# Kernel tuning notes

Hardware: AMD Instinct MI355X
Metric: run time of the kernel (lower is better)

Reference implementation:

```python
import jax, jax.numpy as jnp
import numpy as np

DIM = 1024
NUM_HEADS = 16
HEAD_DIM = DIM // NUM_HEADS
SCALE = HEAD_DIM ** (-0.5)


def setup_inputs() -> dict:
    key = jax.random.key(0)
    ks = jax.random.split(key, 5)
    B, N, C = 2, 2048, DIM
    q = jax.random.normal(ks[0], (B, N, C), dtype=jnp.float32)
    k = jax.random.normal(ks[1], (B, N, C), dtype=jnp.float32)
    v = jax.random.normal(ks[2], (B, N, C), dtype=jnp.float32)
    # fused qkv Linear weight, torch layout [3*C, C]; no bias (qkv_bias=False)
    qkv_w = jax.random.normal(ks[3], (3 * C, C), dtype=jnp.float32) * (C ** -0.5)
    proj_w = jax.random.normal(ks[4], (C, C), dtype=jnp.float32) * (C ** -0.5)
    proj_b = jnp.zeros((C,), dtype=jnp.float32)
    return {"q": q, "k": k, "v": v, "qkv_w": qkv_w, "proj_w": proj_w,
            "proj_b": proj_b, "use_mask": 1}


def reference(q, k, v, qkv_w, proj_w, proj_b, use_mask):
    B, N, C = q.shape
    N_k = k.shape[1]
    H, hd = NUM_HEADS, HEAD_DIM
    # The original applies the full fused qkv Linear to each of q,k,v and keeps
    # only slice 0/1/2 respectively; computing just the used slice is identical math.
    wq, wk, wv = qkv_w[:C], qkv_w[C:2 * C], qkv_w[2 * C:]
    qh = (q @ wq.T).reshape(B, N, H, hd).transpose(0, 2, 1, 3)      # [B,H,N,hd]
    kh = (k @ wk.T).reshape(B, N_k, H, hd).transpose(0, 2, 1, 3)    # [B,H,Nk,hd]
    vh = (v @ wv.T).reshape(B, N_k, H, hd).transpose(0, 2, 1, 3)    # [B,H,Nk,hd]
    attn = jnp.einsum('bhnd,bhmd->bhnm', qh, kh) * SCALE            # [B,H,N,Nk]
    if use_mask:  # static Python flag -> causal tril mask as in the source
        msk = jnp.tril(jnp.ones((N, N_k), dtype=bool))
        attn = jnp.where(msk[None, None], attn, jnp.float32(-1e9))
    attn = jax.nn.softmax(attn, axis=-1)
    x = jnp.einsum('bhnm,bhmd->bhnd', attn, vh)                     # [B,H,N,hd]
    x = x.transpose(0, 2, 1, 3).reshape(B, N, C)
    x = x @ proj_w.T + proj_b
    return x, attn
```

## Files before the change

### kernel.cpp

```cpp
#include <hip/hip_runtime.h>


typedef unsigned short u16;
typedef unsigned int u32;
typedef __attribute__((ext_vector_type(8))) short s16x8;
typedef __attribute__((ext_vector_type(4))) float f32x4;
typedef __attribute__((ext_vector_type(4))) u16 u16x4;

#define AS1 __attribute__((address_space(1)))
#define AS3 __attribute__((address_space(3)))

static __device__ __forceinline__ u16 f2bf(float f) {
  u32 u = __builtin_bit_cast(u32, f);
  u = (u + 0x7fffu + ((u >> 16) & 1u)) >> 16;
  return (u16)u;
}

static __device__ __forceinline__ void gll16(const u16* g, u16* l) {
  __builtin_amdgcn_global_load_lds((const AS1 u32*)g, (AS3 u32*)l, 16, 0, 0);
}

static __device__ __forceinline__ f32x4 mfma_bf16(s16x8 a, s16x8 b, f32x4 c) {
  return __builtin_amdgcn_mfma_f32_16x16x32_bf16(a, b, c, 0, 0, 0);
}

__global__ __launch_bounds__(256) void cast_kernel(const float* __restrict__ in,
                                                   u16* __restrict__ out, int n4) {
  int i = blockIdx.x * 256 + threadIdx.x;
  if (i < n4) {
    f32x4 v = ((const f32x4*)in)[i];
    u16x4 o = { f2bf(v.x), f2bf(v.y), f2bf(v.z), f2bf(v.w) };
    ((u16x4*)out)[i] = o;
  }
}

static __device__ __forceinline__ void gemm_core_1024(
    const u16* __restrict__ A, const u16* __restrict__ Bm,
    int m0, int n0, int t, u16* a_s, u16* b_s, f32x4 acc[4][4]) {
  const int lane = t & 63;
  const int w = t >> 6;
  const int wm = (w & 1) * 64, wn = (w >> 1) * 64;
  const int lrow = lane & 15, lq = lane >> 4;
  const int r0 = t >> 2;
  const int c0 = (t & 3) * 8;

  for (int kt = 0; kt < 1024; kt += 32) {
    __syncthreads();
    gll16(A  + (size_t)(m0 + r0)      * 1024 + kt + c0, &a_s[(size_t)t * 8]);
    gll16(A  + (size_t)(m0 + r0 + 64) * 1024 + kt + c0, &a_s[(size_t)(t + 256) * 8]);
    gll16(Bm + (size_t)(n0 + r0)      * 1024 + kt + c0, &b_s[(size_t)t * 8]);
    gll16(Bm + (size_t)(n0 + r0 + 64) * 1024 + kt + c0, &b_s[(size_t)(t + 256) * 8]);
    __syncthreads();
    s16x8 af[4], bfr[4];
#pragma unroll
    for (int x = 0; x < 4; x++) af[x]  = *(const s16x8*)&a_s[(wm + x*16 + lrow)*32 + lq*8];
#pragma unroll
    for (int x = 0; x < 4; x++) bfr[x] = *(const s16x8*)&b_s[(wn + x*16 + lrow)*32 + lq*8];
#pragma unroll
    for (int tm = 0; tm < 4; tm++)
#pragma unroll
      for (int tn = 0; tn < 4; tn++)
        acc[tm][tn] = mfma_bf16(af[tm], bfr[tn], acc[tm][tn]);
  }
}

__global__ __launch_bounds__(256) void gemm_qkv_kernel(
    const u16* __restrict__ qb, const u16* __restrict__ kb, const u16* __restrict__ vb,
    const u16* __restrict__ wb, u16* __restrict__ Qh, u16* __restrict__ Kh,
    u16* __restrict__ Vt) {
  __shared__ u16 a_s[128*32], b_s[128*32];
  const int mode = blockIdx.z;
  const u16* A = (mode == 0) ? qb : (mode == 1) ? kb : vb;
  const u16* Bm = wb + (size_t)mode * (1024 * 1024);
  const int m0 = blockIdx.y * 128, n0 = blockIdx.x * 128;
  const int t = threadIdx.x;
  f32x4 acc[4][4];
  const f32x4 Z = {0.f, 0.f, 0.f, 0.f};
#pragma unroll
  for (int i = 0; i < 4; i++)
#pragma unroll
    for (int j = 0; j < 4; j++) acc[i][j] = Z;

  gemm_core_1024(A, Bm, m0, n0, t, a_s, b_s, acc);

  const int lane = t & 63, w = t >> 6;
  const int wm = (w & 1) * 64, wn = (w >> 1) * 64;
  const int lrow = lane & 15, lq = lane >> 4;
#pragma unroll
  for (int tm = 0; tm < 4; tm++) {
#pragma unroll
    for (int tn = 0; tn < 4; tn++) {
      const int ng = n0 + wn + tn * 16 + lrow;
      const int h = ng >> 6, d = ng & 63;
#pragma unroll
      for (int i = 0; i < 4; i++) {
        const int mg = m0 + wm + tm * 16 + lq * 4 + i;
        const int b = mg >> 11, s = mg & 2047;
        const float v = acc[tm][tn][i];
        if (mode == 0)
          Qh[((size_t)(b * 16 + h) * 2048 + s) * 64 + d] = f2bf(v * 0.125f);
        else if (mode == 1)
          Kh[((size_t)(b * 16 + h) * 2048 + s) * 64 + d] = f2bf(v);
        else
          Vt[((size_t)(b * 16 + h) * 64 + d) * 2048 + s] = f2bf(v);
      }
    }
  }
}

__global__ __launch_bounds__(256) void gemm_proj_kernel(
    const u16* __restrict__ xatt, const u16* __restrict__ pwb,
    const float* __restrict__ bias, float* __restrict__ out) {
  __shared__ u16 a_s[128*32], b_s[128*32];
  const int m0 = blockIdx.y * 128, n0 = blockIdx.x * 128;
  const int t = threadIdx.x;
  f32x4 acc[4][4];
  const f32x4 Z = {0.f, 0.f, 0.f, 0.f};
#pragma unroll
  for (int i = 0; i < 4; i++)
#pragma unroll
    for (int j = 0; j < 4; j++) acc[i][j] = Z;

  gemm_core_1024(xatt, pwb, m0, n0, t, a_s, b_s, acc);

  const int lane = t & 63, w = t >> 6;
  const int wm = (w & 1) * 64, wn = (w >> 1) * 64;
  const int lrow = lane & 15, lq = lane >> 4;
#pragma unroll
  for (int tn = 0; tn < 4; tn++) {
    const int ng = n0 + wn + tn * 16 + lrow;
    const float bv = bias[ng];
#pragma unroll
    for (int tm = 0; tm < 4; tm++) {
#pragma unroll
      for (int i = 0; i < 4; i++) {
        const int mg = m0 + wm + tm * 16 + lq * 4 + i;
        out[(size_t)mg * 1024 + ng] = acc[tm][tn][i] + bv;
      }
    }
  }
}

__global__ __launch_bounds__(256) void attn_kernel(
    const u16* __restrict__ Qh, const u16* __restrict__ Kh, const u16* __restrict__ Vt,
    float* __restrict__ attn, u16* __restrict__ xatt, const int* __restrict__ use_mask_p) {
  __shared__ u16 q_s[64*64], k_s[64*64], v_s[64*64];
  __shared__ u16 p_s[4][16*64];

  const int bh = blockIdx.y;
  const int q0 = blockIdx.x * 64;
  const int t = threadIdx.x;
  const int lane = t & 63, w = t >> 6;
  const int lrow = lane & 15, lq = lane >> 4;
  const int use_mask = *use_mask_p;
  const int T = use_mask ? (q0 >> 6) : 31;

  const int rs = t >> 3;
  const int cs = (t & 7) * 8;

  const u16* qg = Qh + ((size_t)bh * 2048 + q0) * 64;
  gll16(qg + (size_t)rs * 64 + cs,        &q_s[(size_t)t * 8]);
  gll16(qg + (size_t)(rs + 32) * 64 + cs, &q_s[(size_t)(t + 256) * 8]);
  __syncthreads();

  s16x8 qf[2];
#pragma unroll
  for (int kq = 0; kq < 2; kq++)
    qf[kq] = *(const s16x8*)&q_s[(w * 16 + lrow) * 64 + kq * 32 + lq * 8];

  const u16* kg = Kh + (size_t)bh * (2048 * 64);
  const u16* vg = Vt + (size_t)bh * (64 * 2048);

  float l_acc[4] = {0.f, 0.f, 0.f, 0.f};
  for (int tt = 0; tt <= T; tt++) {
    __syncthreads();
    gll16(kg + (size_t)(tt * 64 + rs) * 64 + cs,      &k_s[(size_t)t * 8]);
    gll16(kg + (size_t)(tt * 64 + rs + 32) * 64 + cs, &k_s[(size_t)(t + 256) * 8]);
    __syncthreads();
    f32x4 sacc[4];
    const f32x4 Z = {0.f, 0.f, 0.f, 0.f};
#pragma unroll
    for (int tn = 0; tn < 4; tn++) {
      sacc[tn] = Z;
#pragma unroll
      for (int kq = 0; kq < 2; kq++) {
        s16x8 kf = *(const s16x8*)&k_s[(tn * 16 + lrow) * 64 + kq * 32 + lq * 8];
        sacc[tn] = mfma_bf16(qf[kq], kf, sacc[tn]);
      }
    }
    const bool diag = use_mask && (tt == T);
    float part[4] = {0.f, 0.f, 0.f, 0.f};
#pragma unroll
    for (int tn = 0; tn < 4; tn++)
#pragma unroll
      for (int i = 0; i < 4; i++) {
        const bool ok = !diag || (tn * 16 + lrow <= w * 16 + lq * 4 + i);
        part[i] += ok ? __expf(sacc[tn][i]) : 0.f;
      }
#pragma unroll
    for (int i = 0; i < 4; i++) {
      float p = part[i];
      p += __shfl_xor(p, 1, 16);
      p += __shfl_xor(p, 2, 16);
      p += __shfl_xor(p, 4, 16);
      p += __shfl_xor(p, 8, 16);
      l_acc[i] += p;
    }
  }
  float inv_l[4];
#pragma unroll
  for (int i = 0; i < 4; i++) inv_l[i] = 1.0f / l_acc[i];

  f32x4 oacc[4];
  const f32x4 Z = {0.f, 0.f, 0.f, 0.f};
#pragma unroll
  for (int i = 0; i < 4; i++) oacc[i] = Z;

  for (int tt = 0; tt <= T; tt++) {
    __syncthreads();
    gll16(kg + (size_t)(tt * 64 + rs) * 64 + cs,      &k_s[(size_t)t * 8]);
    gll16(kg + (size_t)(tt * 64 + rs + 32) * 64 + cs, &k_s[(size_t)(t + 256) * 8]);
    gll16(vg + (size_t)rs * 2048 + tt * 64 + cs,        &v_s[(size_t)t * 8]);
    gll16(vg + (size_t)(rs + 32) * 2048 + tt * 64 + cs, &v_s[(size_t)(t + 256) * 8]);
    __syncthreads();
    f32x4 sacc[4];
#pragma unroll
    for (int tn = 0; tn < 4; tn++) {
      sacc[tn] = Z;
#pragma unroll
      for (int kq = 0; kq < 2; kq++) {
        s16x8 kf = *(const s16x8*)&k_s[(tn * 16 + lrow) * 64 + kq * 32 + lq * 8];
        sacc[tn] = mfma_bf16(qf[kq], kf, sacc[tn]);
      }
    }
    const bool diag = use_mask && (tt == T);
    float* abase = attn + ((size_t)(bh * 2048 + q0 + w * 16)) * 2048 + tt * 64;
#pragma unroll
    for (int tn = 0; tn < 4; tn++)
#pragma unroll
      for (int i = 0; i < 4; i++) {
        const bool ok = !diag || (tn * 16 + lrow <= w * 16 + lq * 4 + i);
        const float p = ok ? __expf(sacc[tn][i]) * inv_l[i] : 0.f;
        const int rl = lq * 4 + i;
        abase[(size_t)rl * 2048 + tn * 16 + lrow] = p;
        p_s[w][rl * 64 + tn * 16 + lrow] = f2bf(p);
      }
    s16x8 pf[2];
#pragma unroll
    for (int kq = 0; kq < 2; kq++)
      pf[kq] = *(const s16x8*)&p_s[w][lrow * 64 + kq * 32 + lq * 8];
#pragma unroll
    for (int td = 0; td < 4; td++)
#pragma unroll
      for (int kq = 0; kq < 2; kq++) {
        s16x8 vf = *(const s16x8*)&v_s[(td * 16 + lrow) * 64 + kq * 32 + lq * 8];
        oacc[td] = mfma_bf16(pf[kq], vf, oacc[td]);
      }
  }

  const int b = bh >> 4, h = bh & 15;
#pragma unroll
  for (int td = 0; td < 4; td++)
#pragma unroll
    for (int i = 0; i < 4; i++) {
      const int row = q0 + w * 16 + lq * 4 + i;
      xatt[((size_t)(b * 2048 + row)) * 1024 + h * 64 + td * 16 + lrow] = f2bf(oacc[td][i]);
    }

  if (use_mask) {
    const int zc0 = q0 + 64;
    if (zc0 < 2048) {
      const int nzv = (2048 - zc0) >> 2;
      f32x4* zb = (f32x4*)(attn + ((size_t)bh * 2048 + q0) * 2048 + zc0);
      const int row = t >> 2;
      const f32x4 Z4 = {0.f, 0.f, 0.f, 0.f};
      for (int c = (t & 3); c < nzv; c += 4)
        zb[(size_t)row * 512 + c] = Z4;
    }
  }
}

extern "C" void kernel_launch(void* const* d_in, const int* in_sizes, int n_in,
                              void* d_out, int out_size, void* d_ws, size_t ws_size,
                              hipStream_t stream) {
  const float* q      = (const float*)d_in[0];
  const float* k      = (const float*)d_in[1];
  const float* v      = (const float*)d_in[2];
  const float* qkv_w  = (const float*)d_in[3];
  const float* proj_w = (const float*)d_in[4];
  const float* proj_b = (const float*)d_in[5];
  const int*   use_mask = (const int*)d_in[6];

  const size_t MB = 1024 * 1024;
  char* ws = (char*)d_ws;
  u16* qb  = (u16*)(ws + 0 * MB);
  u16* kb  = (u16*)(ws + 8 * MB);
  u16* vb  = (u16*)(ws + 16 * MB);
  u16* wb  = (u16*)(ws + 24 * MB);
  u16* pwb = (u16*)(ws + 30 * MB);
  u16* Qh  = (u16*)(ws + 32 * MB);
  u16* Kh  = (u16*)(ws + 40 * MB);
  u16* Vt  = (u16*)(ws + 48 * MB);
  u16* xat = qb;

  float* out_x    = (float*)d_out;
  float* out_attn = out_x + (size_t)2 * 2048 * 1024;

  cast_kernel<<<4096, 256, 0, stream>>>(q, qb, 1048576);
  cast_kernel<<<4096, 256, 0, stream>>>(k, kb, 1048576);
  cast_kernel<<<4096, 256, 0, stream>>>(v, vb, 1048576);
  cast_kernel<<<3072, 256, 0, stream>>>(qkv_w, wb, 786432);
  cast_kernel<<<1024, 256, 0, stream>>>(proj_w, pwb, 262144);

  gemm_qkv_kernel<<<dim3(8, 32, 3), 256, 0, stream>>>(qb, kb, vb, wb, Qh, Kh, Vt);
  attn_kernel<<<dim3(32, 32), 256, 0, stream>>>(Qh, Kh, Vt, out_attn, xat, use_mask);
  gemm_proj_kernel<<<dim3(8, 32), 256, 0, stream>>>(xat, pwb, proj_b, out_x);
}
```

Before: 773.2 us.

## Swizzle LDS layouts, stage QKV epilogue through LDS, merge cast launches

Applies XOR swizzles to the GEMM and attention LDS tiles to reduce bank conflicts on fragment reads. The QKV GEMM epilogue now stages results in shared memory so Q/K/V are written with 16-byte vector stores instead of scattered 2-byte stores, including the transposed V. The attention P tile is kept as padded fp32 in LDS and converted to bf16 when loaded, the masked-zero fill is reorganized so each wave writes whole rows, and the five cast launches are merged into two. These changes add LDS usage and extra barriers in exchange.

Result: no change. 786.1 us (+1.7%).

```diff
diff --git a/kernel.cpp b/kernel.cpp
--- a/kernel.cpp
+++ b/kernel.cpp
@@ -24,8 +24,27 @@
   return __builtin_amdgcn_mfma_f32_16x16x32_bf16(a, b, c, 0, 0, 0);
 }
 
-__global__ __launch_bounds__(256) void cast_kernel(const float* __restrict__ in,
-                                                   u16* __restrict__ out, int n4) {
+__global__ __launch_bounds__(256) void cast3_kernel(
+    const float* __restrict__ a, const float* __restrict__ b, const float* __restrict__ c,
+    u16* __restrict__ oa, u16* __restrict__ ob, u16* __restrict__ oc, int n4) {
+  const int y = blockIdx.y;
+  const float* in = (y == 0) ? a : (y == 1) ? b : c;
+  u16* out = (y == 0) ? oa : (y == 1) ? ob : oc;
+  int i = blockIdx.x * 256 + threadIdx.x;
+  if (i < n4) {
+    f32x4 v = ((const f32x4*)in)[i];
+    u16x4 o = { f2bf(v.x), f2bf(v.y), f2bf(v.z), f2bf(v.w) };
+    ((u16x4*)out)[i] = o;
+  }
+}
+
+__global__ __launch_bounds__(256) void cast2_kernel(
+    const float* __restrict__ w0, u16* __restrict__ o0, int n40,
+    const float* __restrict__ w1, u16* __restrict__ o1, int n41) {
+  const int y = blockIdx.y;
+  const float* in = y ? w1 : w0;
+  u16* out = y ? o1 : o0;
+  const int n4 = y ? n41 : n40;
   int i = blockIdx.x * 256 + threadIdx.x;
   if (i < n4) {
     f32x4 v = ((const f32x4*)in)[i];
@@ -41,21 +60,37 @@
   const int w = t >> 6;
   const int wm = (w & 1) * 64, wn = (w >> 1) * 64;
   const int lrow = lane & 15, lq = lane >> 4;
-  const int r0 = t >> 2;
-  const int c0 = (t & 3) * 8;
+
+  const int Rst = t >> 3;
+  const int qst = (t & 7) ^ (Rst & 7);
+  const int sr = 2 * Rst + (qst >> 2);
+  const int sc = (qst & 3) * 8;
+
+  int a_off[4], b_off[4];
+#pragma unroll
+  for (int x = 0; x < 4; x++) {
+    int ra = wm + x * 16 + lrow;
+    int Ra = ra >> 1;
+    int pa = (((ra & 1) << 2) + lq) ^ (Ra & 7);
+    a_off[x] = Ra * 64 + pa * 8;
+    int rb = wn + x * 16 + lrow;
+    int Rb = rb >> 1;
+    int pb = (((rb & 1) << 2) + lq) ^ (Rb & 7);
+    b_off[x] = Rb * 64 + pb * 8;
+  }
 
   for (int kt = 0; kt < 1024; kt += 32) {
     __syncthreads();
-    gll16(A  + (size_t)(m0 + r0)      * 1024 + kt + c0, &a_s[(size_t)t * 8]);
-    gll16(A  + (size_t)(m0 + r0 + 64) * 1024 + kt + c0, &a_s[(size_t)(t + 256) * 8]);
-    gll16(Bm + (size_t)(n0 + r0)      * 1024 + kt + c0, &b_s[(size_t)t * 8]);
-    gll16(Bm + (size_t)(n0 + r0 + 64) * 1024 + kt + c0, &b_s[(size_t)(t + 256) * 8]);
+    gll16(A  + (size_t)(m0 + sr)      * 1024 + kt + sc, &a_s[(size_t)t * 8]);
+    gll16(A  + (size_t)(m0 + sr + 64) * 1024 + kt + sc, &a_s[(size_t)(t + 256) * 8]);
+    gll16(Bm + (size_t)(n0 + sr)      * 1024 + kt + sc, &b_s[(size_t)t * 8]);
+    gll16(Bm + (size_t)(n0 + sr + 64) * 1024 + kt + sc, &b_s[(size_t)(t + 256) * 8]);
     __syncthreads();
     s16x8 af[4], bfr[4];
 #pragma unroll
-    for (int x = 0; x < 4; x++) af[x]  = *(const s16x8*)&a_s[(wm + x*16 + lrow)*32 + lq*8];
-#pragma unroll
-    for (int x = 0; x < 4; x++) bfr[x] = *(const s16x8*)&b_s[(wn + x*16 + lrow)*32 + lq*8];
+    for (int x = 0; x < 4; x++) af[x]  = *(const s16x8*)&a_s[a_off[x]];
+#pragma unroll
+    for (int x = 0; x < 4; x++) bfr[x] = *(const s16x8*)&b_s[b_off[x]];
 #pragma unroll
     for (int tm = 0; tm < 4; tm++)
 #pragma unroll
@@ -68,7 +103,9 @@
     const u16* __restrict__ qb, const u16* __restrict__ kb, const u16* __restrict__ vb,
     const u16* __restrict__ wb, u16* __restrict__ Qh, u16* __restrict__ Kh,
     u16* __restrict__ Vt) {
-  __shared__ u16 a_s[128*32], b_s[128*32];
+  __shared__ u16 smem[128 * 136];
+  u16* a_s = smem;
+  u16* b_s = smem + 128 * 32;
   const int mode = blockIdx.z;
   const u16* A = (mode == 0) ? qb : (mode == 1) ? kb : vb;
   const u16* Bm = wb + (size_t)mode * (1024 * 1024);
@@ -82,28 +119,40 @@
     for (int j = 0; j < 4; j++) acc[i][j] = Z;
 
   gemm_core_1024(A, Bm, m0, n0, t, a_s, b_s, acc);
+  __syncthreads();
 
   const int lane = t & 63, w = t >> 6;
   const int wm = (w & 1) * 64, wn = (w >> 1) * 64;
   const int lrow = lane & 15, lq = lane >> 4;
-#pragma unroll
-  for (int tm = 0; tm < 4; tm++) {
+  const float scale = (mode == 0) ? 0.125f : 1.0f;
+#pragma unroll
+  for (int tm = 0; tm < 4; tm++)
 #pragma unroll
     for (int tn = 0; tn < 4; tn++) {
-      const int ng = n0 + wn + tn * 16 + lrow;
-      const int h = ng >> 6, d = ng & 63;
+      const int nl = wn + tn * 16 + lrow;
 #pragma unroll
       for (int i = 0; i < 4; i++) {
-        const int mg = m0 + wm + tm * 16 + lq * 4 + i;
-        const int b = mg >> 11, s = mg & 2047;
-        const float v = acc[tm][tn][i];
-        if (mode == 0)
-          Qh[((size_t)(b * 16 + h) * 2048 + s) * 64 + d] = f2bf(v * 0.125f);
-        else if (mode == 1)
-          Kh[((size_t)(b * 16 + h) * 2048 + s) * 64 + d] = f2bf(v);
-        else
-          Vt[((size_t)(b * 16 + h) * 64 + d) * 2048 + s] = f2bf(v);
-      }
+        const int ml = wm + tm * 16 + lq * 4 + i;
+        const u16 bv = f2bf(acc[tm][tn][i] * scale);
+        if (mode < 2) smem[ml * 136 + nl] = bv;
+        else          smem[nl * 136 + ml] = bv;
+      }
+    }
+  __syncthreads();
+  const int ch = t & 15;
+#pragma unroll
+  for (int rep = 0; rep < 8; rep++) {
+    const int r = rep * 16 + (t >> 4);
+    s16x8 val = *(const s16x8*)&smem[r * 136 + ch * 8];
+    if (mode < 2) {
+      const int m = m0 + r, n = n0 + ch * 8;
+      const int b = m >> 11, s = m & 2047, h = n >> 6, d = n & 63;
+      u16* dst = (mode == 0) ? Qh : Kh;
+      *(s16x8*)&dst[((size_t)(b * 16 + h) * 2048 + s) * 64 + d] = val;
+    } else {
+      const int n = n0 + r, m = m0 + ch * 8;
+      const int b = m >> 11, s = m & 2047, h = n >> 6, d = n & 63;
+      *(s16x8*)&Vt[((size_t)(b * 16 + h) * 64 + d) * 2048 + s] = val;
     }
   }
 }
@@ -111,7 +160,7 @@
 __global__ __launch_bounds__(256) void gemm_proj_kernel(
     const u16* __restrict__ xatt, const u16* __restrict__ pwb,
     const float* __restrict__ bias, float* __restrict__ out) {
-  __shared__ u16 a_s[128*32], b_s[128*32];
+  __shared__ u16 a_s[128 * 32], b_s[128 * 32];
   const int m0 = blockIdx.y * 128, n0 = blockIdx.x * 128;
   const int t = threadIdx.x;
   f32x4 acc[4][4];
@@ -144,8 +193,8 @@
 __global__ __launch_bounds__(256) void attn_kernel(
     const u16* __restrict__ Qh, const u16* __restrict__ Kh, const u16* __restrict__ Vt,
     float* __restrict__ attn, u16* __restrict__ xatt, const int* __restrict__ use_mask_p) {
-  __shared__ u16 q_s[64*64], k_s[64*64], v_s[64*64];
-  __shared__ u16 p_s[4][16*64];
+  __shared__ u16 q_s[64 * 64], k_s[64 * 64], v_s[64 * 64];
+  __shared__ float p32[4][16 * 68];
 
   const int bh = blockIdx.y;
   const int q0 = blockIdx.x * 64;
@@ -156,7 +205,9 @@
   const int T = use_mask ? (q0 >> 6) : 31;
 
   const int rs = t >> 3;
-  const int cs = (t & 7) * 8;
+  const int cs = (((t & 7) ^ (rs & 7))) * 8;
+  const int sw0 = ((0 + lq) ^ (lrow & 7)) * 8;
+  const int sw1 = ((4 + lq) ^ (lrow & 7)) * 8;
 
   const u16* qg = Qh + ((size_t)bh * 2048 + q0) * 64;
   gll16(qg + (size_t)rs * 64 + cs,        &q_s[(size_t)t * 8]);
@@ -164,12 +215,12 @@
   __syncthreads();
 
   s16x8 qf[2];
-#pragma unroll
-  for (int kq = 0; kq < 2; kq++)
-    qf[kq] = *(const s16x8*)&q_s[(w * 16 + lrow) * 64 + kq * 32 + lq * 8];
+  qf[0] = *(const s16x8*)&q_s[(w * 16 + lrow) * 64 + sw0];
+  qf[1] = *(const s16x8*)&q_s[(w * 16 + lrow) * 64 + sw1];
 
   const u16* kg = Kh + (size_t)bh * (2048 * 64);
   const u16* vg = Vt + (size_t)bh * (64 * 2048);
+  const f32x4 Z = {0.f, 0.f, 0.f, 0.f};
 
   float l_acc[4] = {0.f, 0.f, 0.f, 0.f};
   for (int tt = 0; tt <= T; tt++) {
@@ -178,15 +229,13 @@
     gll16(kg + (size_t)(tt * 64 + rs + 32) * 64 + cs, &k_s[(size_t)(t + 256) * 8]);
     __syncthreads();
     f32x4 sacc[4];
-    const f32x4 Z = {0.f, 0.f, 0.f, 0.f};
 #pragma unroll
     for (int tn = 0; tn < 4; tn++) {
       sacc[tn] = Z;
-#pragma unroll
-      for (int kq = 0; kq < 2; kq++) {
-        s16x8 kf = *(const s16x8*)&k_s[(tn * 16 + lrow) * 64 + kq * 32 + lq * 8];
-        sacc[tn] = mfma_bf16(qf[kq], kf, sacc[tn]);
-      }
+      s16x8 kf0 = *(const s16x8*)&k_s[(tn * 16 + lrow) * 64 + sw0];
+      sacc[tn] = mfma_bf16(qf[0], kf0, sacc[tn]);
+      s16x8 kf1 = *(const s16x8*)&k_s[(tn * 16 + lrow) * 64 + sw1];
+      sacc[tn] = mfma_bf16(qf[1], kf1, sacc[tn]);
     }
     const bool diag = use_mask && (tt == T);
     float part[4] = {0.f, 0.f, 0.f, 0.f};
@@ -212,14 +261,13 @@
   for (int i = 0; i < 4; i++) inv_l[i] = 1.0f / l_acc[i];
 
   f32x4 oacc[4];
-  const f32x4 Z = {0.f, 0.f, 0.f, 0.f};
 #pragma unroll
   for (int i = 0; i < 4; i++) oacc[i] = Z;
 
   for (int tt = 0; tt <= T; tt++) {
     __syncthreads();
-    gll16(kg + (size_t)(tt * 64 + rs) * 64 + cs,      &k_s[(size_t)t * 8]);
-    gll16(kg + (size_t)(tt * 64 + rs + 32) * 64 + cs, &k_s[(size_t)(t + 256) * 8]);
+    gll16(kg + (size_t)(tt * 64 + rs) * 64 + cs,        &k_s[(size_t)t * 8]);
+    gll16(kg + (size_t)(tt * 64 + rs + 32) * 64 + cs,   &k_s[(size_t)(t + 256) * 8]);
     gll16(vg + (size_t)rs * 2048 + tt * 64 + cs,        &v_s[(size_t)t * 8]);
     gll16(vg + (size_t)(rs + 32) * 2048 + tt * 64 + cs, &v_s[(size_t)(t + 256) * 8]);
     __syncthreads();
@@ -227,11 +275,10 @@
 #pragma unroll
     for (int tn = 0; tn < 4; tn++) {
       sacc[tn] = Z;
-#pragma unroll
-      for (int kq = 0; kq < 2; kq++) {
-        s16x8 kf = *(const s16x8*)&k_s[(tn * 16 + lrow) * 64 + kq * 32 + lq * 8];
-        sacc[tn] = mfma_bf16(qf[kq], kf, sacc[tn]);
-      }
+      s16x8 kf0 = *(const s16x8*)&k_s[(tn * 16 + lrow) * 64 + sw0];
+      sacc[tn] = mfma_bf16(qf[0], kf0, sacc[tn]);
+      s16x8 kf1 = *(const s16x8*)&k_s[(tn * 16 + lrow) * 64 + sw1];
+      sacc[tn] = mfma_bf16(qf[1], kf1, sacc[tn]);
     }
     const bool diag = use_mask && (tt == T);
     float* abase = attn + ((size_t)(bh * 2048 + q0 + w * 16)) * 2048 + tt * 64;
@@ -243,19 +290,23 @@
         const float p = ok ? __expf(sacc[tn][i]) * inv_l[i] : 0.f;
         const int rl = lq * 4 + i;
         abase[(size_t)rl * 2048 + tn * 16 + lrow] = p;
-        p_s[w][rl * 64 + tn * 16 + lrow] = f2bf(p);
-      }
-    s16x8 pf[2];
-#pragma unroll
-    for (int kq = 0; kq < 2; kq++)
-      pf[kq] = *(const s16x8*)&p_s[w][lrow * 64 + kq * 32 + lq * 8];
-#pragma unroll
-    for (int td = 0; td < 4; td++)
-#pragma unroll
-      for (int kq = 0; kq < 2; kq++) {
-        s16x8 vf = *(const s16x8*)&v_s[(td * 16 + lrow) * 64 + kq * 32 + lq * 8];
-        oacc[td] = mfma_bf16(pf[kq], vf, oacc[td]);
-      }
+        p32[w][rl * 68 + tn * 16 + lrow] = p;
+      }
+#pragma unroll
+    for (int kq = 0; kq < 2; kq++) {
+      f32x4 plo = *(const f32x4*)&p32[w][lrow * 68 + kq * 32 + lq * 8];
+      f32x4 phi = *(const f32x4*)&p32[w][lrow * 68 + kq * 32 + lq * 8 + 4];
+      s16x8 pf;
+      pf[0] = (short)f2bf(plo.x); pf[1] = (short)f2bf(plo.y);
+      pf[2] = (short)f2bf(plo.z); pf[3] = (short)f2bf(plo.w);
+      pf[4] = (short)f2bf(phi.x); pf[5] = (short)f2bf(phi.y);
+      pf[6] = (short)f2bf(phi.z); pf[7] = (short)f2bf(phi.w);
+#pragma unroll
+      for (int td = 0; td < 4; td++) {
+        s16x8 vf = *(const s16x8*)&v_s[(td * 16 + lrow) * 64 + (kq ? sw1 : sw0)];
+        oacc[td] = mfma_bf16(pf, vf, oacc[td]);
+      }
+    }
   }
 
   const int b = bh >> 4, h = bh & 15;
@@ -270,12 +321,13 @@
   if (use_mask) {
     const int zc0 = q0 + 64;
     if (zc0 < 2048) {
-      const int nzv = (2048 - zc0) >> 2;
-      f32x4* zb = (f32x4*)(attn + ((size_t)bh * 2048 + q0) * 2048 + zc0);
-      const int row = t >> 2;
+      const int nz4 = (2048 - zc0) >> 2;
       const f32x4 Z4 = {0.f, 0.f, 0.f, 0.f};
-      for (int c = (t & 3); c < nzv; c += 4)
-        zb[(size_t)row * 512 + c] = Z4;
+#pragma unroll 1
+      for (int r = w * 16; r < w * 16 + 16; r++) {
+        f32x4* zrow = (f32x4*)(attn + ((size_t)(bh * 2048 + q0 + r)) * 2048 + zc0);
+        for (int c = lane; c < nz4; c += 64) zrow[c] = Z4;
+      }
     }
   }
 }
@@ -306,11 +358,8 @@
   float* out_x    = (float*)d_out;
   float* out_attn = out_x + (size_t)2 * 2048 * 1024;
 
-  cast_kernel<<<4096, 256, 0, stream>>>(q, qb, 1048576);
-  cast_kernel<<<4096, 256, 0, stream>>>(k, kb, 1048576);
-  cast_kernel<<<4096, 256, 0, stream>>>(v, vb, 1048576);
-  cast_kernel<<<3072, 256, 0, stream>>>(qkv_w, wb, 786432);
-  cast_kernel<<<1024, 256, 0, stream>>>(proj_w, pwb, 262144);
+  cast3_kernel<<<dim3(4096, 3), 256, 0, stream>>>(q, k, v, qb, kb, vb, 1048576);
+  cast2_kernel<<<dim3(3072, 2), 256, 0, stream>>>(qkv_w, wb, 786432, proj_w, pwb, 262144);
 
   gemm_qkv_kernel<<<dim3(8, 32, 3), 256, 0, stream>>>(qb, kb, vb, wb, Qh, Kh, Vt);
   attn_kernel<<<dim3(32, 32), 256, 0, stream>>>(Qh, Kh, Vt, out_attn, xat, use_mask);
```
